# Kernel tuning notes

Measured on AMD Instinct MI355X. Metric: run time of the kernel, lower is better.

Reference implementation:

```python
import jax, jax.numpy as jnp
import numpy as np

N = 50000      # nodes
DEG = 16       # fixed neighbor count per node -> E = N*DEG edges
F_IN = 128
F_OUT = 128


def setup_inputs() -> dict:
    key = jax.random.key(0)
    k = jax.random.split(key, 6)
    E = N * DEG
    x = jax.random.normal(k[0], (N, F_IN), dtype=jnp.float32)
    weight = jax.random.normal(k[1], (F_IN, F_OUT), dtype=jnp.float32) * (1.0 / np.sqrt(F_OUT))
    bias = jax.random.normal(k[2], (F_OUT,), dtype=jnp.float32) * (1.0 / np.sqrt(F_OUT))
    weights_mask = jax.random.normal(k[3], (2 * F_IN, F_IN), dtype=jnp.float32) * (1.0 / np.sqrt(F_IN))
    adj_vals = jax.random.uniform(k[4], (E,), dtype=jnp.float32)
    edge_src = jax.random.randint(k[5], (E,), 0, N, dtype=jnp.int32)   # neighbor ids (add_all flattened)
    edge_dst = jnp.repeat(jnp.arange(N, dtype=jnp.int32), DEG)         # center node ids
    return {"x": x, "weight": weight, "bias": bias, "weights_mask": weights_mask,
            "adj_vals": adj_vals, "edge_src": edge_src, "edge_dst": edge_dst}


def reference(x, weight, bias, weights_mask, adj_vals, edge_src, edge_dst):
    # Per-edge: concat(center, neighbor) -> mask MLP -> sigmoid (dropout omitted: eval mode)
    cen = x[edge_dst]                    # [E, F]
    nei = x[edge_src]                    # [E, F]
    cen_nei = jnp.concatenate([cen, nei], axis=1)          # [E, 2F]
    mask = jax.nn.sigmoid(cen_nei @ weights_mask)          # [E, F]
    # Weighted neighbor sum scattered back to centers, plus self feature
    agg = jax.ops.segment_sum(mask * nei, edge_dst, num_segments=N)   # [N, F]
    x_new = x + agg
    # Dense transform then spmm aggregation (adj given as edge list with values)
    support = x_new @ weight                                # [N, F_out]
    out = jax.ops.segment_sum(adj_vals[:, None] * support[edge_src], edge_dst, num_segments=N)
    return out + bias
```

## Files before the change

### kernel.cpp

```cpp
#include <hip/hip_runtime.h>
#include <stdint.h>
#include <stddef.h>


#define NNODES 50000
#define DEG    16
#define FD     128

#define NEG_LOG2E -1.44269504f

typedef __bf16 bf16x8 __attribute__((ext_vector_type(8)));
typedef short  s16x8  __attribute__((ext_vector_type(8)));
typedef float  f32x4  __attribute__((ext_vector_type(4)));
typedef float  f32x2  __attribute__((ext_vector_type(2)));

__device__ __forceinline__ short f2bf_s(float f) {
    union { float f; uint32_t u; } v; v.f = f;
    uint32_t r = v.u + 0x7fffu + ((v.u >> 16) & 1u);
    return (short)(r >> 16);
}
__device__ __forceinline__ float bflo(uint32_t u) {
    union { uint32_t u; float f; } v; v.u = u << 16;
    return v.f;
}
__device__ __forceinline__ float bfhi(uint32_t u) {
    union { uint32_t u; float f; } v; v.u = u & 0xffff0000u;
    return v.f;
}

__global__ __launch_bounds__(256) void pack_k(const float* __restrict__ wm,
                                              const float* __restrict__ w,
                                              short* __restrict__ wmb,
                                              short* __restrict__ wpack) {
    int tid = blockIdx.x * 256 + threadIdx.x;
    if (tid < 128 * 256) {
        int k = tid >> 8, c = tid & 255;
        float v = (c < 128) ? wm[k * 128 + c] : wm[(128 + k) * 128 + (c - 128)];
        int idx = (((k >> 5) * 16 + (c >> 4)) * 64 + ((k >> 3) & 3) * 16 + (c & 15)) * 8 + (k & 7);
        wmb[idx] = f2bf_s(v);
    }
    if (tid < 128 * 128) {
        int k = tid >> 7, n = tid & 127;
        int idx = (((k >> 5) * 8 + (n >> 4)) * 64 + ((k >> 3) & 3) * 16 + (n & 15)) * 8 + (k & 7);
        wpack[idx] = f2bf_s(w[tid]);
    }
}

__global__ __launch_bounds__(256) void zy_k(const float* __restrict__ x,
                                            const short* __restrict__ wmb,
                                            short* __restrict__ zbf,
                                            uint32_t* __restrict__ xy) {
    const int tid = threadIdx.x, wave = tid >> 6, lane = tid & 63;
    const int q = lane >> 4, m = lane & 15;
    const int node0 = blockIdx.x * 16;

    f32x4 acc[4];
    #pragma unroll
    for (int nt = 0; nt < 4; ++nt) acc[nt] = (f32x4){0.f, 0.f, 0.f, 0.f};

    #pragma unroll
    for (int kk = 0; kk < 4; ++kk) {
        const float* rp = x + (size_t)(node0 + m) * FD + kk * 32 + q * 8;
        f32x4 lo = *reinterpret_cast<const f32x4*>(rp);
        f32x4 hi = *reinterpret_cast<const f32x4*>(rp + 4);
        bf16x8 a;
        a[0]=(__bf16)lo.x; a[1]=(__bf16)lo.y; a[2]=(__bf16)lo.z; a[3]=(__bf16)lo.w;
        a[4]=(__bf16)hi.x; a[5]=(__bf16)hi.y; a[6]=(__bf16)hi.z; a[7]=(__bf16)hi.w;
        #pragma unroll
        for (int nt = 0; nt < 4; ++nt) {
            int frag = kk * 16 + wave * 4 + nt;
            s16x8 braw = *reinterpret_cast<const s16x8*>(wmb + ((size_t)frag * 64 + lane) * 8);
            acc[nt] = __builtin_amdgcn_mfma_f32_16x16x32_bf16(a, __builtin_bit_cast(bf16x8, braw), acc[nt], 0, 0, 0);
        }
    }
    #pragma unroll
    for (int nt = 0; nt < 4; ++nt) {
        int c = (wave * 4 + nt) * 16 + m;
        #pragma unroll
        for (int i = 0; i < 4; ++i) {
            int row = node0 + q * 4 + i;
            float val = NEG_LOG2E * acc[nt][i];
            if (c < 128) {
                zbf[(size_t)row * FD + c] = f2bf_s(val);
            } else {
                int f = c - 128;
                float xv = x[(size_t)row * FD + f];
                uint32_t u = (uint32_t)(uint16_t)f2bf_s(xv) | ((uint32_t)(uint16_t)f2bf_s(val) << 16);
                xy[(size_t)row * FD + f] = u;
            }
        }
    }
}

__global__ __launch_bounds__(256) void edge_k(const short* __restrict__ zbf,
                                              const uint32_t* __restrict__ xy,
                                              const int* __restrict__ esrc,
                                              const short* __restrict__ wpack,
                                              short* __restrict__ support) {
    __shared__ float xn[16 * 132];
    const int tid = threadIdx.x, wave = tid >> 6, lane = tid & 63;
    const int q = lane >> 4, m = lane & 15;
    const int node0 = blockIdx.x * 16;

    #pragma unroll
    for (int mt = 0; mt < 4; ++mt) {
        const int nu = __builtin_amdgcn_readfirstlane(node0 + wave * 4 + mt);
        const int* ep = esrc + nu * DEG;
        uint32_t z2 = reinterpret_cast<const uint32_t*>(zbf + (size_t)nu * FD)[lane];
        float zn0 = bflo(z2), zn1 = bfhi(z2);
        float a0a = 0.f, a0b = 0.f, a1a = 0.f, a1b = 0.f;
        #pragma unroll
        for (int e = 0; e < 16; ++e) {
            int s = ep[e];
            uint2 u = reinterpret_cast<const uint2*>(xy + (size_t)s * FD)[lane];
            float g0 = __builtin_amdgcn_rcpf(1.f + __builtin_amdgcn_exp2f(zn0 + bfhi(u.x)));
            float g1 = __builtin_amdgcn_rcpf(1.f + __builtin_amdgcn_exp2f(zn1 + bfhi(u.y)));
            if (e & 1) { a0b += g0 * bflo(u.x); a1b += g1 * bflo(u.y); }
            else       { a0a += g0 * bflo(u.x); a1a += g1 * bflo(u.y); }
        }
        uint2 c = reinterpret_cast<const uint2*>(xy + (size_t)nu * FD)[lane];
        f32x2 xv;
        xv.x = bflo(c.x) + a0a + a0b;
        xv.y = bflo(c.y) + a1a + a1b;
        *reinterpret_cast<f32x2*>(&xn[(wave * 4 + mt) * 132 + 2 * lane]) = xv;
    }
    __syncthreads();

    f32x4 sacc[2];
    sacc[0] = (f32x4){0.f, 0.f, 0.f, 0.f};
    sacc[1] = (f32x4){0.f, 0.f, 0.f, 0.f};
    #pragma unroll
    for (int kk = 0; kk < 4; ++kk) {
        const float* p = &xn[m * 132 + kk * 32 + q * 8];
        bf16x8 a;
        a[0]=(__bf16)p[0]; a[1]=(__bf16)p[1]; a[2]=(__bf16)p[2]; a[3]=(__bf16)p[3];
        a[4]=(__bf16)p[4]; a[5]=(__bf16)p[5]; a[6]=(__bf16)p[6]; a[7]=(__bf16)p[7];
        #pragma unroll
        for (int t = 0; t < 2; ++t) {
            int nt = wave * 2 + t;
            s16x8 braw = *reinterpret_cast<const s16x8*>(wpack + ((size_t)(kk * 8 + nt) * 64 + lane) * 8);
            sacc[t] = __builtin_amdgcn_mfma_f32_16x16x32_bf16(a, __builtin_bit_cast(bf16x8, braw), sacc[t], 0, 0, 0);
        }
    }
    #pragma unroll
    for (int t = 0; t < 2; ++t) {
        int nt = wave * 2 + t;
        #pragma unroll
        for (int i = 0; i < 4; ++i)
            support[(size_t)(node0 + q * 4 + i) * FD + nt * 16 + m] = f2bf_s(sacc[t][i]);
    }
}

__global__ __launch_bounds__(256) void final_k(const short* __restrict__ support,
                                               const float* __restrict__ adj,
                                               const int* __restrict__ esrc,
                                               const float* __restrict__ bias,
                                               float* __restrict__ out) {
    const int tid = threadIdx.x, wave = tid >> 6, lane = tid & 63;
    const int n0 = blockIdx.x * 8 + wave * 2;
    f32x2 b = *reinterpret_cast<const f32x2*>(bias + 2 * lane);
    #pragma unroll
    for (int t = 0; t < 2; ++t) {
        const int nu = __builtin_amdgcn_readfirstlane(n0 + t);
        const int* ep = esrc + nu * DEG;
        const float* ap = adj + nu * DEG;
        float a0 = b.x, a1 = b.y, c0 = 0.f, c1 = 0.f;
        #pragma unroll
        for (int e = 0; e < 16; ++e) {
            int s = ep[e];
            float w = ap[e];
            uint32_t u = reinterpret_cast<const uint32_t*>(support + (size_t)s * FD)[lane];
            if (e & 1) { c0 += w * bflo(u); c1 += w * bfhi(u); }
            else       { a0 += w * bflo(u); a1 += w * bfhi(u); }
        }
        f32x2 r; r.x = a0 + c0; r.y = a1 + c1;
        *reinterpret_cast<f32x2*>(out + (size_t)nu * FD + 2 * lane) = r;
    }
}

extern "C" void kernel_launch(void* const* d_in, const int* in_sizes, int n_in,
                              void* d_out, int out_size, void* d_ws, size_t ws_size,
                              hipStream_t stream) {
    const float* x      = (const float*)d_in[0];
    const float* weight = (const float*)d_in[1];
    const float* bias   = (const float*)d_in[2];
    const float* wm     = (const float*)d_in[3];
    const float* adj    = (const float*)d_in[4];
    const int*   esrc   = (const int*)d_in[5];

    short*    wmb     = (short*)d_ws;
    short*    wpack   = (short*)((char*)d_ws + 65536);
    short*    zbf     = (short*)((char*)d_ws + 98304);
    short*    support = (short*)((char*)d_ws + 98304 + (size_t)NNODES * FD * 2);
    uint32_t* xy      = (uint32_t*)d_out;
    float*    out     = (float*)d_out;

    pack_k <<<128,         256, 0, stream>>>(wm, weight, wmb, wpack);
    zy_k   <<<NNODES / 16, 256, 0, stream>>>(x, wmb, zbf, xy);
    edge_k <<<NNODES / 16, 256, 0, stream>>>(zbf, xy, esrc, wpack, support);
    final_k<<<NNODES / 8,  256, 0, stream>>>(support, adj, esrc, bias, out);
}
```

Before: 196.8 us.

## Prefetch edge gathers, stage zy output in LDS, widen final gather per wave

Result: no change. 198.1 us (+0.7%).

```diff
diff --git a/kernel.cpp b/kernel.cpp
--- a/kernel.cpp
+++ b/kernel.cpp
@@ -37,7 +37,7 @@
         int k = tid >> 8, c = tid & 255;
         float v = (c < 128) ? wm[k * 128 + c] : wm[(128 + k) * 128 + (c - 128)];
         int idx = (((k >> 5) * 16 + (c >> 4)) * 64 + ((k >> 3) & 3) * 16 + (c & 15)) * 8 + (k & 7);
-        wmb[idx] = f2bf_s(v);
+        wmb[idx] = f2bf_s(NEG_LOG2E * v);
     }
     if (tid < 128 * 128) {
         int k = tid >> 7, n = tid & 127;
@@ -50,6 +50,7 @@
                                             const short* __restrict__ wmb,
                                             short* __restrict__ zbf,
                                             uint32_t* __restrict__ xy) {
+    __shared__ float ct[16 * 260];
     const int tid = threadIdx.x, wave = tid >> 6, lane = tid & 63;
     const int q = lane >> 4, m = lane & 15;
     const int node0 = blockIdx.x * 16;
@@ -74,20 +75,40 @@
         }
     }
     #pragma unroll
-    for (int nt = 0; nt < 4; ++nt) {
-        int c = (wave * 4 + nt) * 16 + m;
-        #pragma unroll
-        for (int i = 0; i < 4; ++i) {
-            int row = node0 + q * 4 + i;
-            float val = NEG_LOG2E * acc[nt][i];
-            if (c < 128) {
-                zbf[(size_t)row * FD + c] = f2bf_s(val);
-            } else {
-                int f = c - 128;
-                float xv = x[(size_t)row * FD + f];
-                uint32_t u = (uint32_t)(uint16_t)f2bf_s(xv) | ((uint32_t)(uint16_t)f2bf_s(val) << 16);
-                xy[(size_t)row * FD + f] = u;
+    for (int nt = 0; nt < 4; ++nt)
+        #pragma unroll
+        for (int i = 0; i < 4; ++i)
+            ct[(q * 4 + i) * 260 + wave * 64 + nt * 16 + m] = acc[nt][i];
+    __syncthreads();
+
+    const int row = tid >> 4;
+    const int c0  = (tid & 15) * 16;
+    const int grow = node0 + row;
+    if (c0 < 128) {
+        uint32_t zo[8];
+        #pragma unroll
+        for (int j = 0; j < 8; ++j) {
+            float v0 = ct[row * 260 + c0 + 2 * j];
+            float v1 = ct[row * 260 + c0 + 2 * j + 1];
+            zo[j] = (uint32_t)(uint16_t)f2bf_s(v0) | ((uint32_t)(uint16_t)f2bf_s(v1) << 16);
+        }
+        uint4* dst = reinterpret_cast<uint4*>(zbf + (size_t)grow * FD + c0);
+        dst[0] = make_uint4(zo[0], zo[1], zo[2], zo[3]);
+        dst[1] = make_uint4(zo[4], zo[5], zo[6], zo[7]);
+    } else {
+        const int f0 = c0 - 128;
+        const float* xr = x + (size_t)grow * FD + f0;
+        uint4* dst = reinterpret_cast<uint4*>(xy + (size_t)grow * FD + f0);
+        #pragma unroll
+        for (int v = 0; v < 4; ++v) {
+            uint32_t xo[4];
+            #pragma unroll
+            for (int j = 0; j < 4; ++j) {
+                float yv = ct[row * 260 + c0 + v * 4 + j];
+                float xv = xr[v * 4 + j];
+                xo[j] = (uint32_t)(uint16_t)f2bf_s(xv) | ((uint32_t)(uint16_t)f2bf_s(yv) << 16);
             }
+            dst[v] = make_uint4(xo[0], xo[1], xo[2], xo[3]);
         }
     }
 }
@@ -101,27 +122,46 @@
     const int tid = threadIdx.x, wave = tid >> 6, lane = tid & 63;
     const int q = lane >> 4, m = lane & 15;
     const int node0 = blockIdx.x * 16;
+    const int nu0 = __builtin_amdgcn_readfirstlane(node0 + wave * 4);
+
+    uint2     buf[2][16];
+    uint2     cr[2];
+    uint32_t  zr[2];
+
+    {
+        const int* ep = esrc + nu0 * DEG;
+        #pragma unroll
+        for (int e = 0; e < 16; ++e)
+            buf[0][e] = reinterpret_cast<const uint2*>(xy + (size_t)ep[e] * FD)[lane];
+        zr[0] = reinterpret_cast<const uint32_t*>(zbf + (size_t)nu0 * FD)[lane];
+        cr[0] = reinterpret_cast<const uint2*>(xy + (size_t)nu0 * FD)[lane];
+    }
 
     #pragma unroll
     for (int mt = 0; mt < 4; ++mt) {
-        const int nu = __builtin_amdgcn_readfirstlane(node0 + wave * 4 + mt);
-        const int* ep = esrc + nu * DEG;
-        uint32_t z2 = reinterpret_cast<const uint32_t*>(zbf + (size_t)nu * FD)[lane];
-        float zn0 = bflo(z2), zn1 = bfhi(z2);
+        const int cur = mt & 1, nxt = cur ^ 1;
+        if (mt < 3) {
+            const int nun = nu0 + mt + 1;
+            const int* ep = esrc + nun * DEG;
+            #pragma unroll
+            for (int e = 0; e < 16; ++e)
+                buf[nxt][e] = reinterpret_cast<const uint2*>(xy + (size_t)ep[e] * FD)[lane];
+            zr[nxt] = reinterpret_cast<const uint32_t*>(zbf + (size_t)nun * FD)[lane];
+            cr[nxt] = reinterpret_cast<const uint2*>(xy + (size_t)nun * FD)[lane];
+        }
+        const float zn0 = bflo(zr[cur]), zn1 = bfhi(zr[cur]);
         float a0a = 0.f, a0b = 0.f, a1a = 0.f, a1b = 0.f;
         #pragma unroll
         for (int e = 0; e < 16; ++e) {
-            int s = ep[e];
-            uint2 u = reinterpret_cast<const uint2*>(xy + (size_t)s * FD)[lane];
+            uint2 u = buf[cur][e];
             float g0 = __builtin_amdgcn_rcpf(1.f + __builtin_amdgcn_exp2f(zn0 + bfhi(u.x)));
             float g1 = __builtin_amdgcn_rcpf(1.f + __builtin_amdgcn_exp2f(zn1 + bfhi(u.y)));
             if (e & 1) { a0b += g0 * bflo(u.x); a1b += g1 * bflo(u.y); }
             else       { a0a += g0 * bflo(u.x); a1a += g1 * bflo(u.y); }
         }
-        uint2 c = reinterpret_cast<const uint2*>(xy + (size_t)nu * FD)[lane];
         f32x2 xv;
-        xv.x = bflo(c.x) + a0a + a0b;
-        xv.y = bflo(c.y) + a1a + a1b;
+        xv.x = bflo(cr[cur].x) + a0a + a0b;
+        xv.y = bflo(cr[cur].y) + a1a + a1b;
         *reinterpret_cast<f32x2*>(&xn[(wave * 4 + mt) * 132 + 2 * lane]) = xv;
     }
     __syncthreads();
@@ -157,24 +197,37 @@
                                                const float* __restrict__ bias,
                                                float* __restrict__ out) {
     const int tid = threadIdx.x, wave = tid >> 6, lane = tid & 63;
-    const int n0 = blockIdx.x * 8 + wave * 2;
+    const int n0 = blockIdx.x * 16 + wave * 4;
     f32x2 b = *reinterpret_cast<const f32x2*>(bias + 2 * lane);
-    #pragma unroll
-    for (int t = 0; t < 2; ++t) {
-        const int nu = __builtin_amdgcn_readfirstlane(n0 + t);
-        const int* ep = esrc + nu * DEG;
-        const float* ap = adj + nu * DEG;
-        float a0 = b.x, a1 = b.y, c0 = 0.f, c1 = 0.f;
-        #pragma unroll
-        for (int e = 0; e < 16; ++e) {
-            int s = ep[e];
-            float w = ap[e];
+
+    int nu[4];
+    const int* ep[4];
+    const float* ap[4];
+    #pragma unroll
+    for (int t = 0; t < 4; ++t) {
+        nu[t] = __builtin_amdgcn_readfirstlane(n0 + t);
+        ep[t] = esrc + nu[t] * DEG;
+        ap[t] = adj + nu[t] * DEG;
+    }
+    float a0[4], a1[4];
+    #pragma unroll
+    for (int t = 0; t < 4; ++t) { a0[t] = b.x; a1[t] = b.y; }
+
+    #pragma unroll
+    for (int e = 0; e < 16; ++e) {
+        #pragma unroll
+        for (int t = 0; t < 4; ++t) {
+            int s = ep[t][e];
+            float w = ap[t][e];
             uint32_t u = reinterpret_cast<const uint32_t*>(support + (size_t)s * FD)[lane];
-            if (e & 1) { c0 += w * bflo(u); c1 += w * bfhi(u); }
-            else       { a0 += w * bflo(u); a1 += w * bfhi(u); }
-        }
-        f32x2 r; r.x = a0 + c0; r.y = a1 + c1;
-        *reinterpret_cast<f32x2*>(out + (size_t)nu * FD + 2 * lane) = r;
+            a0[t] += w * bflo(u);
+            a1[t] += w * bfhi(u);
+        }
+    }
+    #pragma unroll
+    for (int t = 0; t < 4; ++t) {
+        f32x2 r; r.x = a0[t]; r.y = a1[t];
+        *reinterpret_cast<f32x2*>(out + (size_t)nu[t] * FD + 2 * lane) = r;
     }
 }
 
@@ -198,5 +251,5 @@
     pack_k <<<128,         256, 0, stream>>>(wm, weight, wmb, wpack);
     zy_k   <<<NNODES / 16, 256, 0, stream>>>(x, wmb, zbf, xy);
     edge_k <<<NNODES / 16, 256, 0, stream>>>(zbf, xy, esrc, wpack, support);
-    final_k<<<NNODES / 8,  256, 0, stream>>>(support, adj, esrc, bias, out);
-}
+    final_k<<<NNODES / 16, 256, 0, stream>>>(support, adj, esrc, bias, out);
+}
```
